# Optimization experiments

Measured on AMD Instinct MI355X. Metric: run time of the kernel, lower is better.

Reference implementation:

```python
import jax, jax.numpy as jnp
import numpy as np

B, D, OUT = 256, 63, 128
DP = D + 1  # 64


def setup_inputs() -> dict:
    key = jax.random.key(0)
    k1, k2, k3, k4, k5 = jax.random.split(key, 5)
    return {
        "x": jax.random.normal(k1, (B, D), dtype=jnp.float32),
        "protein_output": jax.random.normal(k2, (B, D), dtype=jnp.float32),
        "dynamic_output": jax.random.normal(k3, (B, D), dtype=jnp.float32),
        "W": jax.random.normal(k4, (DP ** 3, OUT), dtype=jnp.float32) * 0.02,
        "b": jax.random.normal(k5, (OUT,), dtype=jnp.float32) * 0.02,
    }


def reference(x, protein_output, dynamic_output, W, b):
    bsz = x.shape[0]
    ones = jnp.ones((bsz, 1), dtype=x.dtype)
    a = jnp.concatenate([x, ones], axis=1)               # [B, D+1]
    p = jnp.concatenate([protein_output, ones], axis=1)   # [B, D+1]
    d = jnp.concatenate([dynamic_output, ones], axis=1)   # [B, D+1]
    # rank-1 trilinear outer product, flattened row-major: idx = (i*(D+1)+j)*(D+1)+k
    ab = jnp.einsum('bi,bj->bij', a, p)                   # [B, D+1, D+1]
    abc = jnp.einsum('bij,bk->bijk', ab, d)               # [B, D+1, D+1, D+1]
    feat = abc.reshape(bsz, -1)                           # [B, (D+1)^3]
    return feat @ W + b                                   # [B, OUT]
```

## Files before the change

kernel.cpp:

```cpp
#include <hip/hip_runtime.h>
#include <hip/hip_bf16.h>

typedef __attribute__((ext_vector_type(8))) short short8v;
typedef __attribute__((ext_vector_type(4))) short short4v;
typedef __attribute__((ext_vector_type(4))) float floatx4;

__device__ __forceinline__ unsigned int pkbf(float a, float b) {
  __hip_bfloat162 h = __float22bfloat162_rn(make_float2(a, b));
  union { __hip_bfloat162 h; unsigned int u; } c; c.h = h;
  return c.u;
}

__global__ void bias_init(const float* __restrict__ bias, float* __restrict__ out) {
  int idx = blockIdx.x * 256 + threadIdx.x;
  out[idx] = bias[idx & 127];
}

__global__ __launch_bounds__(512, 2)
void tfn_gemm(const float* __restrict__ X, const float* __restrict__ P,
              const float* __restrict__ Dyn, const float* __restrict__ W,
              float* __restrict__ out) {
  constexpr int WT_STRIDE = 36;
  __shared__ short Wt[2][128][WT_STRIDE];
  __shared__ float p_lds[256 * 17];

  const int tid = threadIdx.x;
  const int wv = tid >> 6, lane = tid & 63;
  const int q = lane >> 4, l16 = lane & 15;
  const int r = wv & 3;
  const int cg = wv >> 2;

  const int c = blockIdx.x;
  const int i = c >> 2;
  const int j0 = (c & 3) << 4;
  const long gk0 = (long)c << 10;

  for (int idx = tid; idx < 256 * 16; idx += 512) {
    int bb = idx >> 4, jj = idx & 15;
    int j = j0 + jj;
    p_lds[bb * 17 + jj] = (j < 63) ? P[bb * 63 + j] : 1.0f;
  }

  float e[4][2][8];
  #pragma unroll
  for (int rt = 0; rt < 4; ++rt) {
    int brow = (r << 6) + (rt << 4) + l16;
    float av = (i < 63) ? X[brow * 63 + i] : 1.0f;
    #pragma unroll
    for (int h = 0; h < 2; ++h) {
      int kb = (h << 5) + (q << 3);
      #pragma unroll
      for (int t = 0; t < 8; ++t) {
        int k = kb + t;
        float dv = (k < 63) ? Dyn[brow * 63 + k] : 1.0f;
        e[rt][h][t] = av * dv;
      }
    }
  }

  floatx4 acc[4][4];
  #pragma unroll
  for (int a = 0; a < 4; ++a)
    #pragma unroll
    for (int b = 0; b < 4; ++b) acc[a][b] = (floatx4)0.0f;

  const int sn = tid & 127;
  const int skk = (tid >> 7) << 3;

  float w[8];
  {
    const float* wp = W + (gk0 + skk) * 128 + sn;
    #pragma unroll
    for (int u = 0; u < 8; ++u) w[u] = wp[u * 128];
    short* dst = &Wt[0][sn][skk];
    unsigned int* d32 = (unsigned int*)dst;
    d32[0] = pkbf(w[0], w[1]); d32[1] = pkbf(w[2], w[3]);
    d32[2] = pkbf(w[4], w[5]); d32[3] = pkbf(w[6], w[7]);
  }
  __syncthreads();

  for (int jj = 0; jj < 16; ++jj) {
    float pb[4];
    #pragma unroll
    for (int rt = 0; rt < 4; ++rt)
      pb[rt] = p_lds[((r << 6) + (rt << 4) + l16) * 17 + jj];

    #pragma unroll
    for (int h = 0; h < 2; ++h) {
      const int s = (jj << 1) | h;
      const int cur = h;

      if (s < 31) {
        const float* wp = W + (gk0 + (long)(s + 1) * 32 + skk) * 128 + sn;
        #pragma unroll
        for (int u = 0; u < 8; ++u) w[u] = wp[u * 128];
      }

      union { short8v v; short4v hv[2]; } fb[4];
      #pragma unroll
      for (int nt = 0; nt < 4; ++nt) {
        const short* src = &Wt[cur][(cg << 6) + (nt << 4) + l16][q << 3];
        fb[nt].hv[0] = *(const short4v*)src;
        fb[nt].hv[1] = *(const short4v*)(src + 4);
      }

      union { short8v v; unsigned int u[4]; } fa[4];
      #pragma unroll
      for (int rt = 0; rt < 4; ++rt) {
        #pragma unroll
        for (int v2 = 0; v2 < 4; ++v2)
          fa[rt].u[v2] = pkbf(pb[rt] * e[rt][h][2 * v2], pb[rt] * e[rt][h][2 * v2 + 1]);
      }

      #pragma unroll
      for (int rt = 0; rt < 4; ++rt)
        #pragma unroll
        for (int nt = 0; nt < 4; ++nt)
          acc[rt][nt] = __builtin_amdgcn_mfma_f32_16x16x32_bf16(
              fa[rt].v, fb[nt].v, acc[rt][nt], 0, 0, 0);

      if (s < 31) {
        short* dst = &Wt[1 - cur][sn][skk];
        unsigned int* d32 = (unsigned int*)dst;
        d32[0] = pkbf(w[0], w[1]); d32[1] = pkbf(w[2], w[3]);
        d32[2] = pkbf(w[4], w[5]); d32[3] = pkbf(w[6], w[7]);
      }
      __syncthreads();
    }
  }

  #pragma unroll
  for (int rt = 0; rt < 4; ++rt) {
    #pragma unroll
    for (int nt = 0; nt < 4; ++nt) {
      int col = (cg << 6) + (nt << 4) + l16;
      #pragma unroll
      for (int g = 0; g < 4; ++g) {
        int brow = (r << 6) + (rt << 4) + (q << 2) + g;
        atomicAdd(&out[brow * 128 + col], acc[rt][nt][g]);
      }
    }
  }
}

extern "C" void kernel_launch(void* const* d_in, const int* in_sizes, int n_in,
                              void* d_out, int out_size, void* d_ws, size_t ws_size,
                              hipStream_t stream) {
  const float* x   = (const float*)d_in[0];
  const float* p   = (const float*)d_in[1];
  const float* dyn = (const float*)d_in[2];
  const float* W   = (const float*)d_in[3];
  const float* b   = (const float*)d_in[4];
  float* out = (float*)d_out;

  bias_init<<<128, 256, 0, stream>>>(b, out);
  tfn_gemm<<<256, 512, 0, stream>>>(x, p, dyn, W, out);
}
```

Before: 246.6 us.

## Load W fragments directly into registers and replace atomics with split-K partial reduction

Drops the LDS staging of W and the per-step __syncthreads. Each lane now loads its own MFMA B-fragment straight from global memory, with register double-buffering (wA/wB) to overlap loads with compute. The p_lds layout is transposed. The final atomicAdd accumulation into the output is replaced by per-block partial stores to a 32 MB workspace, followed by a separate reduction kernel that adds the bias. The cost is strided uncoalesced global loads of W, extra register pressure, and 32 MB of extra write and read traffic in place of the atomic contention.

```diff
diff --git a/kernel.cpp b/kernel.cpp
--- a/kernel.cpp
+++ b/kernel.cpp
@@ -2,7 +2,6 @@
 #include <hip/hip_bf16.h>
 
 typedef __attribute__((ext_vector_type(8))) short short8v;
-typedef __attribute__((ext_vector_type(4))) short short4v;
 typedef __attribute__((ext_vector_type(4))) float floatx4;
 
 __device__ __forceinline__ unsigned int pkbf(float a, float b) {
@@ -16,13 +15,27 @@
   out[idx] = bias[idx & 127];
 }
 
+__global__ __launch_bounds__(128)
+void reduce_k(const float* __restrict__ part, const float* __restrict__ bias,
+              float* __restrict__ out) {
+  int o = blockIdx.x * 128 + threadIdx.x;
+  const float* p = part + o;
+  float s0 = 0.f, s1 = 0.f, s2 = 0.f, s3 = 0.f;
+  #pragma unroll 8
+  for (int c = 0; c < 256; c += 4) {
+    s0 += p[(long)c * 32768];
+    s1 += p[(long)(c + 1) * 32768];
+    s2 += p[(long)(c + 2) * 32768];
+    s3 += p[(long)(c + 3) * 32768];
+  }
+  out[o] = s0 + s1 + s2 + s3 + bias[o & 127];
+}
+
 __global__ __launch_bounds__(512, 2)
 void tfn_gemm(const float* __restrict__ X, const float* __restrict__ P,
               const float* __restrict__ Dyn, const float* __restrict__ W,
-              float* __restrict__ out) {
-  constexpr int WT_STRIDE = 36;
-  __shared__ short Wt[2][128][WT_STRIDE];
-  __shared__ float p_lds[256 * 17];
+              float* __restrict__ part, float* __restrict__ out, int use_ws) {
+  __shared__ float p_lds[16][256];
 
   const int tid = threadIdx.x;
   const int wv = tid >> 6, lane = tid & 63;
@@ -38,7 +51,7 @@
   for (int idx = tid; idx < 256 * 16; idx += 512) {
     int bb = idx >> 4, jj = idx & 15;
     int j = j0 + jj;
-    p_lds[bb * 17 + jj] = (j < 63) ? P[bb * 63 + j] : 1.0f;
+    p_lds[jj][bb] = (j < 63) ? P[bb * 63 + j] : 1.0f;
   }
 
   float e[4][2][8];
@@ -64,82 +77,106 @@
     #pragma unroll
     for (int b = 0; b < 4; ++b) acc[a][b] = (floatx4)0.0f;
 
-  const int sn = tid & 127;
-  const int skk = (tid >> 7) << 3;
-
-  float w[8];
-  {
-    const float* wp = W + (gk0 + skk) * 128 + sn;
-    #pragma unroll
-    for (int u = 0; u < 8; ++u) w[u] = wp[u * 128];
-    short* dst = &Wt[0][sn][skk];
-    unsigned int* d32 = (unsigned int*)dst;
-    d32[0] = pkbf(w[0], w[1]); d32[1] = pkbf(w[2], w[3]);
-    d32[2] = pkbf(w[4], w[5]); d32[3] = pkbf(w[6], w[7]);
-  }
   __syncthreads();
+
+  const float* wstep = W + (gk0 + (q << 3)) * 128 + (cg << 6) + l16;
+
+  float wA[4][8], wB[4][8];
+
+  #pragma unroll
+  for (int nt = 0; nt < 4; ++nt)
+    #pragma unroll
+    for (int t = 0; t < 8; ++t)
+      wA[nt][t] = wstep[t * 128 + nt * 16];
 
   for (int jj = 0; jj < 16; ++jj) {
     float pb[4];
     #pragma unroll
     for (int rt = 0; rt < 4; ++rt)
-      pb[rt] = p_lds[((r << 6) + (rt << 4) + l16) * 17 + jj];
-
-    #pragma unroll
-    for (int h = 0; h < 2; ++h) {
-      const int s = (jj << 1) | h;
-      const int cur = h;
-
-      if (s < 31) {
-        const float* wp = W + (gk0 + (long)(s + 1) * 32 + skk) * 128 + sn;
-        #pragma unroll
-        for (int u = 0; u < 8; ++u) w[u] = wp[u * 128];
-      }
-
-      union { short8v v; short4v hv[2]; } fb[4];
-      #pragma unroll
-      for (int nt = 0; nt < 4; ++nt) {
-        const short* src = &Wt[cur][(cg << 6) + (nt << 4) + l16][q << 3];
-        fb[nt].hv[0] = *(const short4v*)src;
-        fb[nt].hv[1] = *(const short4v*)(src + 4);
-      }
-
-      union { short8v v; unsigned int u[4]; } fa[4];
-      #pragma unroll
-      for (int rt = 0; rt < 4; ++rt) {
-        #pragma unroll
-        for (int v2 = 0; v2 < 4; ++v2)
-          fa[rt].u[v2] = pkbf(pb[rt] * e[rt][h][2 * v2], pb[rt] * e[rt][h][2 * v2 + 1]);
-      }
-
+      pb[rt] = p_lds[jj][(r << 6) + (rt << 4) + l16];
+
+    {
+      const float* wp = wstep + ((long)(2 * jj + 1) << 12);
+      #pragma unroll
+      for (int nt = 0; nt < 4; ++nt)
+        #pragma unroll
+        for (int t = 0; t < 8; ++t)
+          wB[nt][t] = wp[t * 128 + nt * 16];
+
+      union { short8v v; unsigned int u[4]; } fb[4], fa[4];
+      #pragma unroll
+      for (int nt = 0; nt < 4; ++nt)
+        #pragma unroll
+        for (int v2 = 0; v2 < 4; ++v2)
+          fb[nt].u[v2] = pkbf(wA[nt][2 * v2], wA[nt][2 * v2 + 1]);
+      #pragma unroll
+      for (int rt = 0; rt < 4; ++rt)
+        #pragma unroll
+        for (int v2 = 0; v2 < 4; ++v2)
+          fa[rt].u[v2] = pkbf(pb[rt] * e[rt][0][2 * v2], pb[rt] * e[rt][0][2 * v2 + 1]);
       #pragma unroll
       for (int rt = 0; rt < 4; ++rt)
         #pragma unroll
         for (int nt = 0; nt < 4; ++nt)
           acc[rt][nt] = __builtin_amdgcn_mfma_f32_16x16x32_bf16(
               fa[rt].v, fb[nt].v, acc[rt][nt], 0, 0, 0);
-
-      if (s < 31) {
-        short* dst = &Wt[1 - cur][sn][skk];
-        unsigned int* d32 = (unsigned int*)dst;
-        d32[0] = pkbf(w[0], w[1]); d32[1] = pkbf(w[2], w[3]);
-        d32[2] = pkbf(w[4], w[5]); d32[3] = pkbf(w[6], w[7]);
-      }
-      __syncthreads();
     }
-  }
-
-  #pragma unroll
-  for (int rt = 0; rt < 4; ++rt) {
-    #pragma unroll
-    for (int nt = 0; nt < 4; ++nt) {
-      int col = (cg << 6) + (nt << 4) + l16;
-      #pragma unroll
-      for (int g = 0; g < 4; ++g) {
-        int brow = (r << 6) + (rt << 4) + (q << 2) + g;
-        atomicAdd(&out[brow * 128 + col], acc[rt][nt][g]);
-      }
+
+    {
+      if (jj < 15) {
+        const float* wp = wstep + ((long)(2 * jj + 2) << 12);
+        #pragma unroll
+        for (int nt = 0; nt < 4; ++nt)
+          #pragma unroll
+          for (int t = 0; t < 8; ++t)
+            wA[nt][t] = wp[t * 128 + nt * 16];
+      }
+
+      union { short8v v; unsigned int u[4]; } fb[4], fa[4];
+      #pragma unroll
+      for (int nt = 0; nt < 4; ++nt)
+        #pragma unroll
+        for (int v2 = 0; v2 < 4; ++v2)
+          fb[nt].u[v2] = pkbf(wB[nt][2 * v2], wB[nt][2 * v2 + 1]);
+      #pragma unroll
+      for (int rt = 0; rt < 4; ++rt)
+        #pragma unroll
+        for (int v2 = 0; v2 < 4; ++v2)
+          fa[rt].u[v2] = pkbf(pb[rt] * e[rt][1][2 * v2], pb[rt] * e[rt][1][2 * v2 + 1]);
+      #pragma unroll
+      for (int rt = 0; rt < 4; ++rt)
+        #pragma unroll
+        for (int nt = 0; nt < 4; ++nt)
+          acc[rt][nt] = __builtin_amdgcn_mfma_f32_16x16x32_bf16(
+              fa[rt].v, fb[nt].v, acc[rt][nt], 0, 0, 0);
     }
+  }
+
+  if (use_ws) {
+    float* pt = part + ((long)c << 15);
+    #pragma unroll
+    for (int rt = 0; rt < 4; ++rt)
+      #pragma unroll
+      for (int nt = 0; nt < 4; ++nt) {
+        int col = (cg << 6) + (nt << 4) + l16;
+        #pragma unroll
+        for (int g = 0; g < 4; ++g) {
+          int brow = (r << 6) + (rt << 4) + (q << 2) + g;
+          pt[brow * 128 + col] = acc[rt][nt][g];
+        }
+      }
+  } else {
+    #pragma unroll
+    for (int rt = 0; rt < 4; ++rt)
+      #pragma unroll
+      for (int nt = 0; nt < 4; ++nt) {
+        int col = (cg << 6) + (nt << 4) + l16;
+        #pragma unroll
+        for (int g = 0; g < 4; ++g) {
+          int brow = (r << 6) + (rt << 4) + (q << 2) + g;
+          atomicAdd(&out[brow * 128 + col], acc[rt][nt][g]);
+        }
+      }
   }
 }
 
@@ -153,6 +190,13 @@
   const float* b   = (const float*)d_in[4];
   float* out = (float*)d_out;
 
-  bias_init<<<128, 256, 0, stream>>>(b, out);
-  tfn_gemm<<<256, 512, 0, stream>>>(x, p, dyn, W, out);
-}
+  const size_t need = (size_t)256 * 32768 * sizeof(float);
+  if (d_ws != nullptr && ws_size >= need) {
+    float* part = (float*)d_ws;
+    tfn_gemm<<<256, 512, 0, stream>>>(x, p, dyn, W, part, out, 1);
+    reduce_k<<<256, 128, 0, stream>>>(part, b, out);
+  } else {
+    bias_init<<<128, 256, 0, stream>>>(b, out);
+    tfn_gemm<<<256, 512, 0, stream>>>(x, p, dyn, W, nullptr, out, 0);
+  }
+}
```

Result: faster. 240.6 us (-2.4%).

## Load W fragments directly from global into registers, drop LDS staging and barriers

Applied to the files above, without the earlier changes.

Each wave now reads its own B-operand W fragments straight from global memory into registers, prefetching one step ahead. This removes the shared-memory W double buffer and the per-step __syncthreads. The p_lds layout is transposed to [16][256], and the atomicAdd order is rotated per block to spread contention. In exchange, the four row-group waves in a block each fetch the same W tile, so global/L2 traffic rises about fourfold and register pressure grows from holding 64 prefetched floats per thread.

```diff
diff --git a/kernel.cpp b/kernel.cpp
--- a/kernel.cpp
+++ b/kernel.cpp
@@ -2,7 +2,6 @@
 #include <hip/hip_bf16.h>
 
 typedef __attribute__((ext_vector_type(8))) short short8v;
-typedef __attribute__((ext_vector_type(4))) short short4v;
 typedef __attribute__((ext_vector_type(4))) float floatx4;
 
 __device__ __forceinline__ unsigned int pkbf(float a, float b) {
@@ -20,9 +19,7 @@
 void tfn_gemm(const float* __restrict__ X, const float* __restrict__ P,
               const float* __restrict__ Dyn, const float* __restrict__ W,
               float* __restrict__ out) {
-  constexpr int WT_STRIDE = 36;
-  __shared__ short Wt[2][128][WT_STRIDE];
-  __shared__ float p_lds[256 * 17];
+  __shared__ float p_lds[16][256];
 
   const int tid = threadIdx.x;
   const int wv = tid >> 6, lane = tid & 63;
@@ -38,7 +35,7 @@
   for (int idx = tid; idx < 256 * 16; idx += 512) {
     int bb = idx >> 4, jj = idx & 15;
     int j = j0 + jj;
-    p_lds[bb * 17 + jj] = (j < 63) ? P[bb * 63 + j] : 1.0f;
+    p_lds[jj][bb] = (j < 63) ? P[bb * 63 + j] : 1.0f;
   }
 
   float e[4][2][8];
@@ -64,75 +61,84 @@
     #pragma unroll
     for (int b = 0; b < 4; ++b) acc[a][b] = (floatx4)0.0f;
 
-  const int sn = tid & 127;
-  const int skk = (tid >> 7) << 3;
+  __syncthreads();
 
-  float w[8];
-  {
-    const float* wp = W + (gk0 + skk) * 128 + sn;
+  const float* wstep = W + (gk0 + (q << 3)) * 128 + (cg << 6) + l16;
+  const float* wp0 = wstep;
+  const float* wp1 = wstep + 4096;
+
+  float wf0[4][8], wf1[4][8];
+
+  #pragma unroll
+  for (int nt = 0; nt < 4; ++nt)
     #pragma unroll
-    for (int u = 0; u < 8; ++u) w[u] = wp[u * 128];
-    short* dst = &Wt[0][sn][skk];
-    unsigned int* d32 = (unsigned int*)dst;
-    d32[0] = pkbf(w[0], w[1]); d32[1] = pkbf(w[2], w[3]);
-    d32[2] = pkbf(w[4], w[5]); d32[3] = pkbf(w[6], w[7]);
+    for (int t = 0; t < 8; ++t) {
+      wf0[nt][t] = wp0[t * 128 + nt * 16];
+      wf1[nt][t] = wp1[t * 128 + nt * 16];
+    }
+
+#define FA_MFMA(h, fbv)                                                         \
+  {                                                                             \
+    union { short8v v; unsigned int u[4]; } fa[4];                              \
+    _Pragma("unroll") for (int rt = 0; rt < 4; ++rt)                            \
+        _Pragma("unroll") for (int v2 = 0; v2 < 4; ++v2)                        \
+            fa[rt].u[v2] = pkbf(pb[rt] * e[rt][h][2 * v2],                      \
+                                pb[rt] * e[rt][h][2 * v2 + 1]);                 \
+    _Pragma("unroll") for (int rt = 0; rt < 4; ++rt)                            \
+        _Pragma("unroll") for (int nt = 0; nt < 4; ++nt)                        \
+            acc[rt][nt] = __builtin_amdgcn_mfma_f32_16x16x32_bf16(              \
+                fa[rt].v, (fbv)[nt].v, acc[rt][nt], 0, 0, 0);                   \
   }
-  __syncthreads();
 
   for (int jj = 0; jj < 16; ++jj) {
     float pb[4];
     #pragma unroll
     for (int rt = 0; rt < 4; ++rt)
-      pb[rt] = p_lds[((r << 6) + (rt << 4) + l16) * 17 + jj];
+      pb[rt] = p_lds[jj][(r << 6) + (rt << 4) + l16];
 
+    union { short8v v; unsigned int u[4]; } fb0[4];
     #pragma unroll
-    for (int h = 0; h < 2; ++h) {
-      const int s = (jj << 1) | h;
-      const int cur = h;
+    for (int nt = 0; nt < 4; ++nt)
+      #pragma unroll
+      for (int v2 = 0; v2 < 4; ++v2)
+        fb0[nt].u[v2] = pkbf(wf0[nt][2 * v2], wf0[nt][2 * v2 + 1]);
+    if (jj < 15) {
+      const float* np = wp0 + 8192;
+      #pragma unroll
+      for (int nt = 0; nt < 4; ++nt)
+        #pragma unroll
+        for (int t = 0; t < 8; ++t)
+          wf0[nt][t] = np[t * 128 + nt * 16];
+    }
+    FA_MFMA(0, fb0)
 
-      if (s < 31) {
-        const float* wp = W + (gk0 + (long)(s + 1) * 32 + skk) * 128 + sn;
+    union { short8v v; unsigned int u[4]; } fb1[4];
+    #pragma unroll
+    for (int nt = 0; nt < 4; ++nt)
+      #pragma unroll
+      for (int v2 = 0; v2 < 4; ++v2)
+        fb1[nt].u[v2] = pkbf(wf1[nt][2 * v2], wf1[nt][2 * v2 + 1]);
+    if (jj < 15) {
+      const float* np = wp1 + 8192;
+      #pragma unroll
+      for (int nt = 0; nt < 4; ++nt)
         #pragma unroll
-        for (int u = 0; u < 8; ++u) w[u] = wp[u * 128];
-      }
+        for (int t = 0; t < 8; ++t)
+          wf1[nt][t] = np[t * 128 + nt * 16];
+    }
+    FA_MFMA(1, fb1)
 
-      union { short8v v; short4v hv[2]; } fb[4];
-      #pragma unroll
-      for (int nt = 0; nt < 4; ++nt) {
-        const short* src = &Wt[cur][(cg << 6) + (nt << 4) + l16][q << 3];
-        fb[nt].hv[0] = *(const short4v*)src;
-        fb[nt].hv[1] = *(const short4v*)(src + 4);
-      }
-
-      union { short8v v; unsigned int u[4]; } fa[4];
-      #pragma unroll
-      for (int rt = 0; rt < 4; ++rt) {
-        #pragma unroll
-        for (int v2 = 0; v2 < 4; ++v2)
-          fa[rt].u[v2] = pkbf(pb[rt] * e[rt][h][2 * v2], pb[rt] * e[rt][h][2 * v2 + 1]);
-      }
-
-      #pragma unroll
-      for (int rt = 0; rt < 4; ++rt)
-        #pragma unroll
-        for (int nt = 0; nt < 4; ++nt)
-          acc[rt][nt] = __builtin_amdgcn_mfma_f32_16x16x32_bf16(
-              fa[rt].v, fb[nt].v, acc[rt][nt], 0, 0, 0);
-
-      if (s < 31) {
-        short* dst = &Wt[1 - cur][sn][skk];
-        unsigned int* d32 = (unsigned int*)dst;
-        d32[0] = pkbf(w[0], w[1]); d32[1] = pkbf(w[2], w[3]);
-        d32[2] = pkbf(w[4], w[5]); d32[3] = pkbf(w[6], w[7]);
-      }
-      __syncthreads();
-    }
+    wp0 += 8192;
+    wp1 += 8192;
   }
+#undef FA_MFMA
 
   #pragma unroll
-  for (int rt = 0; rt < 4; ++rt) {
+  for (int rt0 = 0; rt0 < 4; ++rt0) {
     #pragma unroll
-    for (int nt = 0; nt < 4; ++nt) {
+    for (int nt0 = 0; nt0 < 4; ++nt0) {
+      const int rt = (rt0 + (c >> 2)) & 3;
+      const int nt = (nt0 + c) & 3;
       int col = (cg << 6) + (nt << 4) + l16;
       #pragma unroll
       for (int g = 0; g < 4; ++g) {
```

New measurement: 251.9 us. +2.2%, slower.
